# Kernel tuning notes

Measured on AMD Instinct MI355X. Metric: run time of the kernel, lower is better.

The kernel has to match this reference:

```python
import jax, jax.numpy as jnp
import numpy as np

N_DELTA, N_THETA, N_GAMMA = 8, 16, 64
HIDDEN = 64
N_STEPS = 20
DT = 0.01
K_INTRA = 1.0   # within-band Kuramoto coupling
K_CROSS = 0.5   # slow-band -> fast-band drive
TWO_PI = 2.0 * np.pi


def _lin(key, fan_in, fan_out):
    s = 1.0 / np.sqrt(fan_in)
    kw, kb = jax.random.split(key)
    w = jax.random.uniform(kw, (fan_in, fan_out), jnp.float32, -s, s)
    b = jax.random.uniform(kb, (fan_out,), jnp.float32, -s, s)
    return w, b


def setup_inputs() -> dict:
    key = jax.random.key(0)
    ks = jax.random.split(key, 12)
    B, N, D_SCENE, D_QUERY = 65536, 8, 16, 60
    scene = jax.random.normal(ks[0], (B, N, D_SCENE), jnp.float32)
    query = jax.random.normal(ks[1], (B, D_QUERY), jnp.float32)
    # per-sample seeded initial oscillator state (phases uniform, band-typical freqs in Hz)
    delta_phase0 = jax.random.uniform(ks[2], (B, N_DELTA), jnp.float32, 0.0, TWO_PI)
    theta_phase0 = jax.random.uniform(ks[3], (B, N_THETA), jnp.float32, 0.0, TWO_PI)
    gamma_phase0 = jax.random.uniform(ks[4], (B, N_GAMMA), jnp.float32, 0.0, TWO_PI)
    delta_freq = jax.random.uniform(ks[5], (B, N_DELTA), jnp.float32, 1.0, 4.0)
    theta_freq = jax.random.uniform(ks[6], (B, N_THETA), jnp.float32, 4.0, 8.0)
    gamma_freq = jax.random.uniform(ks[7], (B, N_GAMMA), jnp.float32, 30.0, 80.0)
    scene_w, scene_b = _lin(ks[8], D_SCENE, N_GAMMA)
    query_w, query_b = _lin(ks[9], D_QUERY, HIDDEN)
    total_osc = N_DELTA + N_THETA + N_GAMMA
    ro_w1, ro_b1 = _lin(ks[10], total_osc + HIDDEN, HIDDEN)
    ro_w2, ro_b2 = _lin(ks[11], HIDDEN, 2)
    return dict(scene=scene, query=query,
                delta_phase0=delta_phase0, theta_phase0=theta_phase0, gamma_phase0=gamma_phase0,
                delta_freq=delta_freq, theta_freq=theta_freq, gamma_freq=gamma_freq,
                scene_w=scene_w, scene_b=scene_b, query_w=query_w, query_b=query_b,
                ro_w1=ro_w1, ro_b1=ro_b1, ro_w2=ro_w2, ro_b2=ro_b2)


def _meanfield(p, a):
    # mean_j a_j*sin(p_j - p_i) computed in O(n) via sin/cos decomposition
    s = jnp.mean(a * jnp.sin(p), axis=-1, keepdims=True)
    c = jnp.mean(a * jnp.cos(p), axis=-1, keepdims=True)
    return jnp.cos(p) * s - jnp.sin(p) * c


def _cross(p_slow, a_slow, p_fast):
    s = jnp.mean(a_slow * jnp.sin(p_slow), axis=-1, keepdims=True)
    c = jnp.mean(a_slow * jnp.cos(p_slow), axis=-1, keepdims=True)
    return jnp.cos(p_fast) * s - jnp.sin(p_fast) * c


def _integrate(pd, ad, pt, at, pg, ag, fd, ft, fg):
    def step(carry, _):
        pd, ad, pt, at, pg, ag = carry
        dpd = TWO_PI * fd + K_INTRA * _meanfield(pd, ad)
        dpt = TWO_PI * ft + K_INTRA * _meanfield(pt, at) + K_CROSS * _cross(pd, ad, pt)
        dpg = TWO_PI * fg + K_INTRA * _meanfield(pg, ag) + K_CROSS * _cross(pt, at, pg)
        dad = ad * (1.0 - ad * ad)   # Stuart-Landau amplitude relaxation
        dat = at * (1.0 - at * at)
        dag = ag * (1.0 - ag * ag)
        new = (pd + DT * dpd, ad + DT * dad,
               pt + DT * dpt, at + DT * dat,
               pg + DT * dpg, ag + DT * dag)
        return new, None
    (pd, ad, pt, at, pg, ag), _ = jax.lax.scan(step, (pd, ad, pt, at, pg, ag), None, length=N_STEPS)
    return ad, at, ag


def reference(scene, query, delta_phase0, theta_phase0, gamma_phase0,
              delta_freq, theta_freq, gamma_freq,
              scene_w, scene_b, query_w, query_b, ro_w1, ro_b1, ro_w2, ro_b2):
    scene_flat = jnp.mean(scene, axis=1)                       # (B, D_scene)
    gamma_init = jax.nn.sigmoid(scene_flat @ scene_w + scene_b)  # (B, n_gamma)
    gamma_init = jax.lax.stop_gradient(gamma_init)             # .detach() in original
    B = scene.shape[0]
    ad0 = jnp.ones((B, N_DELTA), scene.dtype)
    at0 = jnp.ones((B, N_THETA), scene.dtype)
    ad, at, ag = _integrate(delta_phase0, ad0, theta_phase0, at0,
                            gamma_phase0, gamma_init,
                            delta_freq, theta_freq, gamma_freq)
    osc_feat = jnp.concatenate([ad, at, ag], axis=-1)          # (B, 88)
    q_feat = query @ query_w + query_b                         # (B, hidden)
    combined = jnp.concatenate([osc_feat, q_feat], axis=-1)    # (B, 152)
    h = jax.nn.relu(combined @ ro_w1 + ro_b1)
    logits = h @ ro_w2 + ro_b2
    return jax.nn.log_softmax(logits, axis=-1)
```

## Files before the change

### kernel.cpp

```cpp
#include <hip/hip_runtime.h>


typedef __attribute__((ext_vector_type(8))) short short8;
typedef __attribute__((ext_vector_type(4))) float f32x4;

__device__ __forceinline__ unsigned short f2bf(float f) {
  unsigned u = __float_as_uint(f);
  return (unsigned short)((u + 0x7FFFu + ((u >> 16) & 1u)) >> 16);
}
__device__ __forceinline__ float bf2f(unsigned short s) {
  return __uint_as_float(((unsigned)s) << 16);
}

#define WS_WQ    0
#define WS_BEFF  3840
#define WS_WHF   3904
#define WS_WLF   8000

__global__ __launch_bounds__(256) void dtg_prep(
    const float* __restrict__ qw, const float* __restrict__ qb,
    const float* __restrict__ w1, const float* __restrict__ b1,
    float* __restrict__ ws)
{
  __shared__ float sm[256];
  const int blk = blockIdx.x, tid = threadIdx.x;
  const int c = tid & 63, p = tid >> 6;
  if (blk < 60) {
    float acc = 0.f;
    for (int j = p * 16; j < p * 16 + 16; ++j)
      acc = fmaf(qw[blk * 64 + j], w1[(88 + j) * 64 + c], acc);
    sm[tid] = acc;
    __syncthreads();
    if (tid < 64)
      ws[WS_WQ + blk * 64 + tid] = sm[tid] + sm[64 + tid] + sm[128 + tid] + sm[192 + tid];
  } else {
    float acc = 0.f;
    if (p == 0) {
      acc = b1[c];
      for (int r = 0; r < 24; ++r) acc += w1[r * 64 + c];
    }
    for (int j = p * 16; j < p * 16 + 16; ++j)
      acc = fmaf(qb[j], w1[(88 + j) * 64 + c], acc);
    sm[tid] = acc;
    __syncthreads();
    if (tid < 64)
      ws[WS_BEFF + tid] = sm[tid] + sm[64 + tid] + sm[128 + tid] + sm[192 + tid];
  }
}

__global__ __launch_bounds__(64) void dtg_prep2(
    const float* __restrict__ w1, float* __restrict__ ws)
{
  const int frag = blockIdx.x;
  const int lane = threadIdx.x;
  const int idx  = frag * 64 + lane;
  const int nt = frag >> 2, kk = frag & 3;
  const int n = nt * 16 + (lane & 15), q = lane >> 4;
  unsigned short* dh = (unsigned short*)(ws + WS_WHF);
  unsigned short* dl = (unsigned short*)(ws + WS_WLF);
  unsigned short hh[8], ll[8];
#pragma unroll
  for (int j = 0; j < 8; ++j) {
    const int k = kk * 32 + q * 8 + j;
    float w;
    if      (k < 60)  w = ws[WS_WQ + k * 64 + n];
    else if (k < 124) w = w1[(24 + k - 60) * 64 + n];
    else              w = 0.f;
    hh[j] = f2bf(w);
    ll[j] = f2bf(w - bf2f(hh[j]));
  }
#pragma unroll
  for (int j = 0; j < 8; ++j) { dh[idx * 8 + j] = hh[j]; dl[idx * 8 + j] = ll[j]; }
}

#define XH_OFF 0
#define XL_OFF 8704
#define SF_OFF 13312
#define L_BYTES (13312 + 16*36*4)

#define KSTEP(ACC, XV, WV)                                                     \
  { const float x_[4] = {(XV).x, (XV).y, (XV).z, (XV).w};                      \
    const float w_[4] = {(WV).x, (WV).y, (WV).z, (WV).w};                      \
    _Pragma("unroll") for (int si_ = 0; si_ < 4; ++si_)                        \
      _Pragma("unroll") for (int ci_ = 0; ci_ < 4; ++ci_)                      \
        ACC[si_][ci_] = fmaf(x_[si_], w_[ci_], ACC[si_][ci_]); }

__global__ __launch_bounds__(128, 4) void dtg_main(
    const float* __restrict__ scene,
    const float* __restrict__ query,
    const float* __restrict__ sw,
    const float* __restrict__ sb,
    const float* __restrict__ w2,
    const float* __restrict__ b2,
    const float* __restrict__ ws,
    float* __restrict__ outf)
{
  __shared__ __align__(16) char smem[L_BYTES];
  const int tid = threadIdx.x;
  const int blk = blockIdx.x;
  float* sf = (float*)(smem + SF_OFF);

  {
    const int s = tid >> 2, q = tid & 3;
    const float4* sp = (const float4*)scene + (size_t)blk * 1024;
    float4 a = make_float4(0.f, 0.f, 0.f, 0.f);
#pragma unroll
    for (int n = 0; n < 8; ++n) {
      float4 v = sp[s * 32 + n * 4 + q];
      a.x += v.x; a.y += v.y; a.z += v.z; a.w += v.w;
    }
    sf[(4 * q + 0) * 36 + s] = a.x * 0.125f;
    sf[(4 * q + 1) * 36 + s] = a.y * 0.125f;
    sf[(4 * q + 2) * 36 + s] = a.z * 0.125f;
    sf[(4 * q + 3) * 36 + s] = a.w * 0.125f;

    const float4* qp = (const float4*)query + (size_t)blk * 480;
#pragma unroll
    for (int m = 0; m < 4; ++m) {
      const int f4i = q + 4 * m;
      if (f4i < 15) {
        float4 v = qp[s * 15 + f4i];
        const float xs[4] = {v.x, v.y, v.z, v.w};
        unsigned short h[4], l[4];
#pragma unroll
        for (int j = 0; j < 4; ++j) {
          h[j] = f2bf(xs[j]);
          l[j] = f2bf(xs[j] - bf2f(h[j]));
        }
        uint2 ph, pl;
        ph.x = (unsigned)h[0] | ((unsigned)h[1] << 16);
        ph.y = (unsigned)h[2] | ((unsigned)h[3] << 16);
        pl.x = (unsigned)l[0] | ((unsigned)l[1] << 16);
        pl.y = (unsigned)l[2] | ((unsigned)l[3] << 16);
        *(uint2*)(smem + XH_OFF + s * 272 + f4i * 8) = ph;
        *(uint2*)(smem + XL_OFF + s * 144 + f4i * 8) = pl;
      }
    }
    if (tid < 32) {
      *(uint2*)(smem + XH_OFF + tid * 272 + 248) = make_uint2(0u, 0u);
      *(uint2*)(smem + XL_OFF + tid * 144 + 120) = make_uint2(0u, 0u);
    }
  }
  __syncthreads();

  const int sgrp = tid >> 4, cgrp = tid & 15;
  {
    float ga[4][4];
    float4 bsv = ((const float4*)sb)[cgrp];
#pragma unroll
    for (int si = 0; si < 4; ++si) {
      ga[si][0] = bsv.x; ga[si][1] = bsv.y; ga[si][2] = bsv.z; ga[si][3] = bsv.w;
    }
    const float4* swp = (const float4*)sw;
#pragma unroll 4
    for (int k = 0; k < 16; ++k) {
      float4 xv = *(const float4*)(sf + k * 36 + 4 * sgrp);
      float4 wv = swp[k * 16 + cgrp];
      KSTEP(ga, xv, wv)
    }
#pragma unroll
    for (int si = 0; si < 4; ++si)
#pragma unroll
      for (int ci = 0; ci < 4; ++ci)
        ga[si][ci] = __builtin_amdgcn_rcpf(1.f + __expf(-ga[si][ci]));
    for (int st = 0; st < 20; ++st) {
#pragma unroll
      for (int si = 0; si < 4; ++si)
#pragma unroll
        for (int ci = 0; ci < 4; ++ci) {
          float a = ga[si][ci];
          ga[si][ci] = fmaf(0.01f, a - a * a * a, a);
        }
    }
#pragma unroll
    for (int si = 0; si < 4; ++si) {
      uint2 pw;
      pw.x = (unsigned)f2bf(ga[si][0]) | ((unsigned)f2bf(ga[si][1]) << 16);
      pw.y = (unsigned)f2bf(ga[si][2]) | ((unsigned)f2bf(ga[si][3]) << 16);
      *(uint2*)(smem + XH_OFF + (4 * sgrp + si) * 272 + 120 + 8 * cgrp) = pw;
    }
  }
  __syncthreads();

  const int wv   = tid >> 6, lane = tid & 63;
  const int quad = lane >> 4;
  const int mrow = wv * 16 + (lane & 15);
  const char* arow = smem + XH_OFF + mrow * 272 + quad * 16;
  short8 Ah0 = *(const short8*)(arow + 0);
  short8 Ah1 = *(const short8*)(arow + 64);
  short8 Ah2 = *(const short8*)(arow + 128);
  short8 Ah3 = *(const short8*)(arow + 192);
  const char* lrow = smem + XL_OFF + mrow * 144 + quad * 16;
  short8 Al0 = *(const short8*)(lrow + 0);
  short8 Al1 = *(const short8*)(lrow + 64);

  float  be[4];
  float2 w2v4[4];
#pragma unroll
  for (int nt = 0; nt < 4; ++nt) {
    const int col = nt * 16 + (lane & 15);
    be[nt]   = ws[WS_BEFF + col];
    w2v4[nt] = ((const float2*)w2)[col];
  }

  const short8* bhp = (const short8*)(ws + WS_WHF) + lane;
  const short8* blp = (const short8*)(ws + WS_WLF) + lane;
  short8 c0 = bhp[0], c1 = bhp[64], c2 = bhp[128], c3 = bhp[192];
  short8 c4 = blp[0], c5 = blp[64];

  float l0[4] = {0.f, 0.f, 0.f, 0.f}, l1[4] = {0.f, 0.f, 0.f, 0.f};
#pragma unroll
  for (int nt = 0; nt < 4; ++nt) {
    short8 n0 = c0, n1 = c1, n2 = c2, n3 = c3, n4 = c4, n5 = c5;
    if (nt < 3) {
      const short8* nh = bhp + 256;
      const short8* nl = blp + 256;
      n0 = nh[0]; n1 = nh[64]; n2 = nh[128]; n3 = nh[192];
      n4 = nl[0]; n5 = nl[64];
    }
    f32x4 acc = {0.f, 0.f, 0.f, 0.f};
    acc = __builtin_amdgcn_mfma_f32_16x16x32_bf16(Ah0, c0, acc, 0, 0, 0);
    acc = __builtin_amdgcn_mfma_f32_16x16x32_bf16(Ah1, c1, acc, 0, 0, 0);
    acc = __builtin_amdgcn_mfma_f32_16x16x32_bf16(Ah2, c2, acc, 0, 0, 0);
    acc = __builtin_amdgcn_mfma_f32_16x16x32_bf16(Ah3, c3, acc, 0, 0, 0);
    acc = __builtin_amdgcn_mfma_f32_16x16x32_bf16(Ah0, c4, acc, 0, 0, 0);
    acc = __builtin_amdgcn_mfma_f32_16x16x32_bf16(Ah1, c5, acc, 0, 0, 0);
    acc = __builtin_amdgcn_mfma_f32_16x16x32_bf16(Al0, c0, acc, 0, 0, 0);
    acc = __builtin_amdgcn_mfma_f32_16x16x32_bf16(Al1, c1, acc, 0, 0, 0);
    {
      const short8* bh2p = bhp;
      const short8* bl2p = blp;
      short8 x4 = bl2p[128], x5 = bl2p[192];
      acc = __builtin_amdgcn_mfma_f32_16x16x32_bf16(Ah2, x4, acc, 0, 0, 0);
      acc = __builtin_amdgcn_mfma_f32_16x16x32_bf16(Ah3, x5, acc, 0, 0, 0);
      (void)bh2p;
    }
#pragma unroll
    for (int r = 0; r < 4; ++r) {
      float h = fmaxf(acc[r] + be[nt], 0.f);
      l0[r] = fmaf(h, w2v4[nt].x, l0[r]);
      l1[r] = fmaf(h, w2v4[nt].y, l1[r]);
    }
    bhp += 256; blp += 256;
    c0 = n0; c1 = n1; c2 = n2; c3 = n3; c4 = n4; c5 = n5;
  }
#pragma unroll
  for (int m = 1; m < 16; m <<= 1) {
#pragma unroll
    for (int r = 0; r < 4; ++r) {
      l0[r] += __shfl_xor(l0[r], m);
      l1[r] += __shfl_xor(l1[r], m);
    }
  }
  if ((lane & 15) == 0) {
    const float bb0 = b2[0], bb1 = b2[1];
    float rr[8];
#pragma unroll
    for (int r = 0; r < 4; ++r) {
      float a0 = l0[r] + bb0, a1 = l1[r] + bb1;
      float mx  = fmaxf(a0, a1);
      float e0  = __expf(a0 - mx), e1 = __expf(a1 - mx);
      float lse = mx + __logf(e0 + e1);
      rr[2 * r] = a0 - lse; rr[2 * r + 1] = a1 - lse;
    }
    const int base = blk * 32 + wv * 16 + quad * 4;
    float4* op = (float4*)(outf + base * 2);
    op[0] = make_float4(rr[0], rr[1], rr[2], rr[3]);
    op[1] = make_float4(rr[4], rr[5], rr[6], rr[7]);
  }
}

extern "C" void kernel_launch(void* const* d_in, const int* in_sizes, int n_in,
                              void* d_out, int out_size, void* d_ws, size_t ws_size,
                              hipStream_t stream)
{
  const float* scene = (const float*)d_in[0];
  const float* query = (const float*)d_in[1];
  const float* sw = (const float*)d_in[8];
  const float* sb = (const float*)d_in[9];
  const float* qw = (const float*)d_in[10];
  const float* qb = (const float*)d_in[11];
  const float* w1 = (const float*)d_in[12];
  const float* b1 = (const float*)d_in[13];
  const float* w2 = (const float*)d_in[14];
  const float* b2 = (const float*)d_in[15];
  float* ws = (float*)d_ws;
  const int B = in_sizes[0] / 128;

  hipLaunchKernelGGL(dtg_prep,  dim3(61), dim3(256), 0, stream, qw, qb, w1, b1, ws);
  hipLaunchKernelGGL(dtg_prep2, dim3(16), dim3(64),  0, stream, w1, ws);
  hipLaunchKernelGGL(dtg_main,  dim3(B / 32), dim3(128), 0, stream,
                     scene, query, sw, sb, w2, b2, ws, (float*)d_out);
}
```

Measured before the change: 145.5 us.

## Merge weight-prep kernels into one launch and pack gamma math into float2

Folds the query-weight fold (qw @ w1 slice) into the bf16 hi/lo fragment packing kernel, so the two prep kernels become one five-block launch with no intermediate ws round trip. The goal is to drop one kernel launch and the serial dependency between the prep stages. In the main kernel the scene projection and the 20-step gamma amplitude recurrence are rewritten with 2-wide float vectors, which may let the compiler emit packed FP32 instructions. The two remaining B-fragment loads are also hoisted ahead of the MFMA chain. Each prep thread now does a serial 64-step dot product over 8 outputs, which lengthens that launch.

New measurement: 149.1 us. +2.5%, slower.

```diff
diff --git a/kernel.cpp b/kernel.cpp
--- a/kernel.cpp
+++ b/kernel.cpp
@@ -3,6 +3,7 @@
 
 typedef __attribute__((ext_vector_type(8))) short short8;
 typedef __attribute__((ext_vector_type(4))) float f32x4;
+typedef __attribute__((ext_vector_type(2))) float f32x2;
 
 __device__ __forceinline__ unsigned short f2bf(float f) {
   unsigned u = __float_as_uint(f);
@@ -12,7 +13,6 @@
   return __uint_as_float(((unsigned)s) << 16);
 }
 
-#define WS_WQ    0
 #define WS_BEFF  3840
 #define WS_WHF   3904
 #define WS_WLF   8000
@@ -24,16 +24,8 @@
 {
   __shared__ float sm[256];
   const int blk = blockIdx.x, tid = threadIdx.x;
-  const int c = tid & 63, p = tid >> 6;
-  if (blk < 60) {
-    float acc = 0.f;
-    for (int j = p * 16; j < p * 16 + 16; ++j)
-      acc = fmaf(qw[blk * 64 + j], w1[(88 + j) * 64 + c], acc);
-    sm[tid] = acc;
-    __syncthreads();
-    if (tid < 64)
-      ws[WS_WQ + blk * 64 + tid] = sm[tid] + sm[64 + tid] + sm[128 + tid] + sm[192 + tid];
-  } else {
+  if (blk == 0) {
+    const int c = tid & 63, p = tid >> 6;
     float acc = 0.f;
     if (p == 0) {
       acc = b1[c];
@@ -45,45 +37,46 @@
     __syncthreads();
     if (tid < 64)
       ws[WS_BEFF + tid] = sm[tid] + sm[64 + tid] + sm[128 + tid] + sm[192 + tid];
-  }
-}
-
-__global__ __launch_bounds__(64) void dtg_prep2(
-    const float* __restrict__ w1, float* __restrict__ ws)
-{
-  const int frag = blockIdx.x;
-  const int lane = threadIdx.x;
-  const int idx  = frag * 64 + lane;
-  const int nt = frag >> 2, kk = frag & 3;
-  const int n = nt * 16 + (lane & 15), q = lane >> 4;
-  unsigned short* dh = (unsigned short*)(ws + WS_WHF);
-  unsigned short* dl = (unsigned short*)(ws + WS_WLF);
-  unsigned short hh[8], ll[8];
-#pragma unroll
-  for (int j = 0; j < 8; ++j) {
-    const int k = kk * 32 + q * 8 + j;
-    float w;
-    if      (k < 60)  w = ws[WS_WQ + k * 64 + n];
-    else if (k < 124) w = w1[(24 + k - 60) * 64 + n];
-    else              w = 0.f;
-    hh[j] = f2bf(w);
-    ll[j] = f2bf(w - bf2f(hh[j]));
-  }
-#pragma unroll
-  for (int j = 0; j < 8; ++j) { dh[idx * 8 + j] = hh[j]; dl[idx * 8 + j] = ll[j]; }
+  } else {
+    const int frag = (blk - 1) * 4 + (tid >> 6);
+    const int lane = tid & 63;
+    const int idx  = frag * 64 + lane;
+    const int nt = frag >> 2, kk = frag & 3;
+    const int n = nt * 16 + (lane & 15), q = lane >> 4;
+    const int k0 = kk * 32 + q * 8;
+    float dot[8] = {0.f, 0.f, 0.f, 0.f, 0.f, 0.f, 0.f, 0.f};
+    if (k0 < 60) {
+      for (int j2 = 0; j2 < 64; ++j2) {
+        const float wc = w1[(88 + j2) * 64 + n];
+#pragma unroll
+        for (int j = 0; j < 8; ++j) {
+          const int k  = k0 + j;
+          const int kc = (k < 60) ? k : 0;
+          dot[j] = fmaf(qw[kc * 64 + j2], wc, dot[j]);
+        }
+      }
+    }
+    unsigned short* dh = (unsigned short*)(ws + WS_WHF);
+    unsigned short* dl = (unsigned short*)(ws + WS_WLF);
+#pragma unroll
+    for (int j = 0; j < 8; ++j) {
+      const int k = k0 + j;
+      float w;
+      if      (k < 60)  w = dot[j];
+      else if (k < 124) w = w1[(24 + k - 60) * 64 + n];
+      else              w = 0.f;
+      const unsigned short h = f2bf(w);
+      const unsigned short l = f2bf(w - bf2f(h));
+      dh[idx * 8 + j] = h;
+      dl[idx * 8 + j] = l;
+    }
+  }
 }
 
 #define XH_OFF 0
 #define XL_OFF 8704
 #define SF_OFF 13312
 #define L_BYTES (13312 + 16*36*4)
-
-#define KSTEP(ACC, XV, WV)                                                     \
-  { const float x_[4] = {(XV).x, (XV).y, (XV).z, (XV).w};                      \
-    const float w_[4] = {(WV).x, (WV).y, (WV).z, (WV).w};                      \
-    _Pragma("unroll") for (int si_ = 0; si_ < 4; ++si_)                        \
-      _Pragma("unroll") for (int ci_ = 0; ci_ < 4; ++ci_)                      \
-        ACC[si_][ci_] = fmaf(x_[si_], w_[ci_], ACC[si_][ci_]); }
 
 __global__ __launch_bounds__(128, 4) void dtg_main(
     const float* __restrict__ scene,
@@ -145,38 +138,51 @@
 
   const int sgrp = tid >> 4, cgrp = tid & 15;
   {
-    float ga[4][4];
+    f32x2 ga[4][2];
     float4 bsv = ((const float4*)sb)[cgrp];
-#pragma unroll
-    for (int si = 0; si < 4; ++si) {
-      ga[si][0] = bsv.x; ga[si][1] = bsv.y; ga[si][2] = bsv.z; ga[si][3] = bsv.w;
-    }
+    const f32x2 b01 = {bsv.x, bsv.y};
+    const f32x2 b23 = {bsv.z, bsv.w};
+#pragma unroll
+    for (int si = 0; si < 4; ++si) { ga[si][0] = b01; ga[si][1] = b23; }
     const float4* swp = (const float4*)sw;
 #pragma unroll 4
     for (int k = 0; k < 16; ++k) {
       float4 xv = *(const float4*)(sf + k * 36 + 4 * sgrp);
       float4 wv = swp[k * 16 + cgrp];
-      KSTEP(ga, xv, wv)
+      const f32x2 w01 = {wv.x, wv.y};
+      const f32x2 w23 = {wv.z, wv.w};
+      const float xs[4] = {xv.x, xv.y, xv.z, xv.w};
+#pragma unroll
+      for (int si = 0; si < 4; ++si) {
+        const f32x2 xb = {xs[si], xs[si]};
+        ga[si][0] += xb * w01;
+        ga[si][1] += xb * w23;
+      }
     }
 #pragma unroll
     for (int si = 0; si < 4; ++si)
 #pragma unroll
-      for (int ci = 0; ci < 4; ++ci)
-        ga[si][ci] = __builtin_amdgcn_rcpf(1.f + __expf(-ga[si][ci]));
+      for (int cp = 0; cp < 2; ++cp) {
+        ga[si][cp].x = __builtin_amdgcn_rcpf(1.f + __expf(-ga[si][cp].x));
+        ga[si][cp].y = __builtin_amdgcn_rcpf(1.f + __expf(-ga[si][cp].y));
+      }
+    const f32x2 c01 = {0.01f, 0.01f};
     for (int st = 0; st < 20; ++st) {
 #pragma unroll
       for (int si = 0; si < 4; ++si)
 #pragma unroll
-        for (int ci = 0; ci < 4; ++ci) {
-          float a = ga[si][ci];
-          ga[si][ci] = fmaf(0.01f, a - a * a * a, a);
+        for (int cp = 0; cp < 2; ++cp) {
+          const f32x2 a = ga[si][cp];
+          const f32x2 t = a * a;
+          const f32x2 d = a - t * a;
+          ga[si][cp] = c01 * d + a;
         }
     }
 #pragma unroll
     for (int si = 0; si < 4; ++si) {
       uint2 pw;
-      pw.x = (unsigned)f2bf(ga[si][0]) | ((unsigned)f2bf(ga[si][1]) << 16);
-      pw.y = (unsigned)f2bf(ga[si][2]) | ((unsigned)f2bf(ga[si][3]) << 16);
+      pw.x = (unsigned)f2bf(ga[si][0].x) | ((unsigned)f2bf(ga[si][0].y) << 16);
+      pw.y = (unsigned)f2bf(ga[si][1].x) | ((unsigned)f2bf(ga[si][1].y) << 16);
       *(uint2*)(smem + XH_OFF + (4 * sgrp + si) * 272 + 120 + 8 * cgrp) = pw;
     }
   }
@@ -218,6 +224,7 @@
       n0 = nh[0]; n1 = nh[64]; n2 = nh[128]; n3 = nh[192];
       n4 = nl[0]; n5 = nl[64];
     }
+    short8 x4 = blp[128], x5 = blp[192];
     f32x4 acc = {0.f, 0.f, 0.f, 0.f};
     acc = __builtin_amdgcn_mfma_f32_16x16x32_bf16(Ah0, c0, acc, 0, 0, 0);
     acc = __builtin_amdgcn_mfma_f32_16x16x32_bf16(Ah1, c1, acc, 0, 0, 0);
@@ -227,14 +234,8 @@
     acc = __builtin_amdgcn_mfma_f32_16x16x32_bf16(Ah1, c5, acc, 0, 0, 0);
     acc = __builtin_amdgcn_mfma_f32_16x16x32_bf16(Al0, c0, acc, 0, 0, 0);
     acc = __builtin_amdgcn_mfma_f32_16x16x32_bf16(Al1, c1, acc, 0, 0, 0);
-    {
-      const short8* bh2p = bhp;
-      const short8* bl2p = blp;
-      short8 x4 = bl2p[128], x5 = bl2p[192];
-      acc = __builtin_amdgcn_mfma_f32_16x16x32_bf16(Ah2, x4, acc, 0, 0, 0);
-      acc = __builtin_amdgcn_mfma_f32_16x16x32_bf16(Ah3, x5, acc, 0, 0, 0);
-      (void)bh2p;
-    }
+    acc = __builtin_amdgcn_mfma_f32_16x16x32_bf16(Ah2, x4, acc, 0, 0, 0);
+    acc = __builtin_amdgcn_mfma_f32_16x16x32_bf16(Ah3, x5, acc, 0, 0, 0);
 #pragma unroll
     for (int r = 0; r < 4; ++r) {
       float h = fmaxf(acc[r] + be[nt], 0.f);
@@ -287,8 +288,7 @@
   float* ws = (float*)d_ws;
   const int B = in_sizes[0] / 128;
 
-  hipLaunchKernelGGL(dtg_prep,  dim3(61), dim3(256), 0, stream, qw, qb, w1, b1, ws);
-  hipLaunchKernelGGL(dtg_prep2, dim3(16), dim3(64),  0, stream, w1, ws);
-  hipLaunchKernelGGL(dtg_main,  dim3(B / 32), dim3(128), 0, stream,
+  hipLaunchKernelGGL(dtg_prep, dim3(5), dim3(256), 0, stream, qw, qb, w1, b1, ws);
+  hipLaunchKernelGGL(dtg_main, dim3(B / 32), dim3(128), 0, stream,
                      scene, query, sw, sb, w2, b2, ws, (float*)d_out);
 }
```
